# Optimization experiments

Measured on AMD Instinct MI355X. Metric: run time of the kernel, lower is better.

The kernel has to match this reference:

```python
import jax, jax.numpy as jnp
import numpy as np

EMBED_DIM = 1024
N_HEADS = 16


def setup_inputs() -> dict:
    key = jax.random.key(0)
    k1, k2, k3 = jax.random.split(key, 3)
    B, T, C = 4, 2048, EMBED_DIM
    x0 = jax.random.normal(k1, (B, T, C), dtype=jnp.float32)
    # Linear weights stored as (in, out) so y = x @ W, matching torch Linear math.
    w_attn = jax.random.normal(k2, (C, 3 * C), dtype=jnp.float32) * (1.0 / np.sqrt(C))
    w_proj = jax.random.normal(k3, (C, C), dtype=jnp.float32) * (1.0 / np.sqrt(C))
    return {"x0": x0, "w_attn": w_attn, "w_proj": w_proj}


def reference(x0, w_attn, w_proj):
    B, T, C = x0.shape
    H = N_HEADS
    D = C // H  # head dim
    qkv = x0 @ w_attn                      # [B, T, 3C]
    q, k, v = jnp.split(qkv, 3, axis=-1)
    # [B, T, C] -> [B, H, T, D]
    q = q.reshape(B, T, H, D).transpose(0, 2, 1, 3)
    k = k.reshape(B, T, H, D).transpose(0, 2, 1, 3)
    v = v.reshape(B, T, H, D).transpose(0, 2, 1, 3)
    scale = 1.0 / np.sqrt(D)
    attn = jnp.einsum('bhqd,bhkd->bhqk', q, k) * scale  # [B, H, T, T]
    causal = jnp.tril(jnp.ones((T, T), dtype=bool))
    attn = jnp.where(causal[None, None, :, :], attn, -jnp.inf)
    attn = jax.nn.softmax(attn, axis=-1)
    y = jnp.einsum('bhqk,bhkd->bhqd', attn, v)           # [B, H, T, D]
    y = y.transpose(0, 2, 1, 3).reshape(B, T, C)
    return y @ w_proj
```

## Files before the change

kernel.cpp:

```cpp
#include <hip/hip_runtime.h>

#define TSEQ 2048
#define NB 4
#define NH 16
#define HD 64
#define CEMB 1024
#define MROWS (NB*TSEQ)

typedef _Float16 half8 __attribute__((ext_vector_type(8)));
typedef _Float16 half4_t __attribute__((ext_vector_type(4)));
typedef float floatx4 __attribute__((ext_vector_type(4)));

__device__ __forceinline__ floatx4 mfma16x32(half8 a, half8 b, floatx4 c) {
    return __builtin_amdgcn_mfma_f32_16x16x32_f16(a, b, c, 0, 0, 0);
}

__device__ __forceinline__ void async16(const _Float16* g, _Float16* l) {
    __builtin_amdgcn_global_load_lds((const __attribute__((address_space(1))) void*)g,
                                     (__attribute__((address_space(3))) void*)l, 16, 0, 0);
}

__global__ __launch_bounds__(256) void cvt_fp32_fp16(const float* __restrict__ in,
                                                     _Float16* __restrict__ out) {
    size_t i = ((size_t)blockIdx.x * 256 + threadIdx.x) * 8;
    float4 a = *(const float4*)(in + i);
    float4 b = *(const float4*)(in + i + 4);
    half8 h;
    h[0] = (_Float16)a.x; h[1] = (_Float16)a.y; h[2] = (_Float16)a.z; h[3] = (_Float16)a.w;
    h[4] = (_Float16)b.x; h[5] = (_Float16)b.y; h[6] = (_Float16)b.z; h[7] = (_Float16)b.w;
    *(half8*)(out + i) = h;
}

__global__ __launch_bounds__(256) void transpose_cvt(const float* __restrict__ in,
                                                     _Float16* __restrict__ out,
                                                     int R, int Ccols) {
    __shared__ float tile[32][33];
    int bx = blockIdx.x;
    int by = blockIdx.y;
    int tx = threadIdx.x, ty = threadIdx.y;
    int x = bx * 32 + tx;
#pragma unroll
    for (int i = 0; i < 32; i += 8) {
        int y = by * 32 + ty + i;
        tile[ty + i][tx] = in[(size_t)y * Ccols + x];
    }
    __syncthreads();
#pragma unroll
    for (int i = 0; i < 32; i += 8) {
        int oc = bx * 32 + ty + i;
        int orow = by * 32 + tx;
        out[(size_t)oc * R + orow] = (_Float16)tile[tx][ty + i];
    }
}

template<int MODE>
__global__ __launch_bounds__(256, 2) void gemm_w4(const _Float16* __restrict__ A,
                                                  const _Float16* __restrict__ Bt,
                                                  float* __restrict__ Cf,
                                                  _Float16* __restrict__ Ch,
                                                  _Float16* __restrict__ VTh,
                                                  int N, int K) {
    __shared__ __align__(16) _Float16 As[3][128 * 32];
    __shared__ __align__(16) _Float16 Bs[3][256 * 32];

    const int tid = threadIdx.x;
    const int wv = tid >> 6, lane = tid & 63;
    const int l16 = lane & 15, quad = lane >> 4;

    const int pid = blockIdx.x + gridDim.x * blockIdx.y;
    const int nn = gridDim.y;
    const int pig = 8 * nn;
    const int gid = pid / pig;
    const int rem = pid - gid * pig;
    const int bm = gid * 8 + (rem & 7);
    const int bn = rem >> 3;

    const int rA = tid >> 2;
    const int kA = ((tid & 3) ^ ((tid >> 3) & 3)) * 8;
    const _Float16* Ag = A  + (size_t)(bm * 128 + rA) * K + kA;
    const _Float16* Bg = Bt + (size_t)(bn * 256 + rA) * K + kA;

    auto stage = [&](int slot, int ss) {
        const int k0 = ss * 32;
#pragma unroll
        for (int u = 0; u < 2; u++)
            async16(Ag + (size_t)(u * 64) * K + k0, &As[slot][tid * 8 + u * 2048]);
#pragma unroll
        for (int u = 0; u < 4; u++)
            async16(Bg + (size_t)(u * 64) * K + k0, &Bs[slot][tid * 8 + u * 2048]);
    };

    const floatx4 zero = {0.f, 0.f, 0.f, 0.f};
    floatx4 acc[8][4];
#pragma unroll
    for (int i = 0; i < 8; i++)
#pragma unroll
        for (int j = 0; j < 4; j++) acc[i][j] = zero;

    const int sw2 = (quad ^ ((l16 >> 1) & 3)) * 8;
    const int offA = l16 * 32 + sw2;
    const int offB = (wv * 64 + l16) * 32 + sw2;

#define PHASE(s, slot, slot2, STG, WAIT)                                        \
    do {                                                                        \
        if (STG) stage(slot2, (s) + 2);                                         \
        half8 af[8], bf[4];                                                     \
        _Pragma("unroll") for (int i_ = 0; i_ < 8; i_++)                        \
            af[i_] = *(const half8*)&As[slot][offA + i_ * 512];                 \
        _Pragma("unroll") for (int j_ = 0; j_ < 4; j_++)                        \
            bf[j_] = *(const half8*)&Bs[slot][offB + j_ * 512];                 \
        __builtin_amdgcn_s_setprio(1);                                          \
        _Pragma("unroll") for (int i_ = 0; i_ < 8; i_++)                        \
            _Pragma("unroll") for (int j_ = 0; j_ < 4; j_++)                    \
                acc[i_][j_] = mfma16x32(af[i_], bf[j_], acc[i_][j_]);           \
        __builtin_amdgcn_s_setprio(0);                                          \
        if (WAIT == 2)                                                          \
            asm volatile("s_waitcnt vmcnt(6) lgkmcnt(0)\n\ts_barrier" ::: "memory"); \
        else if (WAIT == 1)                                                     \
            asm volatile("s_waitcnt vmcnt(0) lgkmcnt(0)\n\ts_barrier" ::: "memory"); \
        __builtin_amdgcn_sched_barrier(0);                                      \
    } while (0)

    stage(0, 0); stage(1, 1); stage(2, 2);
    asm volatile("s_waitcnt vmcnt(12)\n\ts_barrier" ::: "memory");

    for (int it = 0; it < 10; ++it) {
        const int s0 = it * 3;
        PHASE(s0 + 0, 0, 2, 1, 2);
        PHASE(s0 + 1, 1, 0, 1, 2);
        PHASE(s0 + 2, 2, 1, 1, 2);
    }
    PHASE(30, 0, 0, 0, 1);
    PHASE(31, 1, 0, 0, 0);
#undef PHASE

    if (MODE == 1) {
#pragma unroll
        for (int i = 0; i < 8; i++) {
            int row = bm * 128 + i * 16 + quad * 4;
#pragma unroll
            for (int j = 0; j < 4; j++) {
                int col = bn * 256 + wv * 64 + j * 16 + l16;
#pragma unroll
                for (int r = 0; r < 4; r++)
                    Cf[(size_t)(row + r) * N + col] = acc[i][j][r];
            }
        }
    } else {
        const int which = bn >> 2;
        if (which < 2) {
#pragma unroll
            for (int j = 0; j < 4; j++) {
                int n = bn * 256 + wv * 64 + j * 16 + l16;
                int c = n & 1023, h = c >> 6, d = c & 63;
                _Float16* dst = Ch + (size_t)which * ((size_t)MROWS * CEMB)
                                   + (size_t)h * (TSEQ * HD) + d;
#pragma unroll
                for (int i = 0; i < 8; i++) {
                    int row = bm * 128 + i * 16 + quad * 4;
#pragma unroll
                    for (int r = 0; r < 4; r++) {
                        int m = row + r;
                        int b = m >> 11, t = m & 2047;
                        dst[(size_t)b * (NH * TSEQ * HD) + (size_t)t * HD] = (_Float16)acc[i][j][r];
                    }
                }
            }
        } else {
#pragma unroll
            for (int j = 0; j < 4; j++) {
                int n = bn * 256 + wv * 64 + j * 16 + l16;
                int c = n & 1023, h = c >> 6, d = c & 63;
#pragma unroll
                for (int i = 0; i < 8; i++) {
                    int m0 = bm * 128 + i * 16 + quad * 4;
                    int b = m0 >> 11, t = m0 & 2047;
                    half4_t pk;
#pragma unroll
                    for (int r = 0; r < 4; r++) pk[r] = (_Float16)acc[i][j][r];
                    *(half4_t*)&VTh[(((size_t)(b * NH + h)) * HD + d) * TSEQ + t] = pk;
                }
            }
        }
    }
}

__global__ __launch_bounds__(512, 4) void attn_fwd(const _Float16* __restrict__ Qg,
                                                   const _Float16* __restrict__ Kg,
                                                   const _Float16* __restrict__ VTg,
                                                   _Float16* __restrict__ Y) {
    __shared__ __align__(16) _Float16 Ks[2][4096];
    __shared__ __align__(16) _Float16 Vt[2][4096];

    const int tid = threadIdx.x;
    const int w = tid >> 6, lane = tid & 63;
    const int l16 = lane & 15, quad = lane >> 4;
    const int bh = blockIdx.y;
    const int x = blockIdx.x;
    const int b = bh >> 4, h = bh & 15;
    const int qt = (b < 2) ? x : (7 - x);

    const _Float16* Qb = Qg + (size_t)bh * TSEQ * HD;
    const _Float16* Kb = Kg + (size_t)bh * TSEQ * HD;
    const _Float16* Vb = VTg + (size_t)bh * HD * TSEQ;

    const _Float16 ksc = (_Float16)(0.125f * 1.44269504089f);
    const floatx4 zero = {0.f, 0.f, 0.f, 0.f};

    half8 qf[2][2];
#pragma unroll
    for (int g = 0; g < 2; g++) {
        const _Float16* qrow = Qb + (size_t)(qt * 256 + g * 128 + w * 16 + l16) * HD;
        qf[g][0] = *(const half8*)(qrow + quad * 8);
        qf[g][1] = *(const half8*)(qrow + 32 + quad * 8);
#pragma unroll
        for (int e = 0; e < 8; e++) { qf[g][0][e] *= ksc; qf[g][1][e] *= ksc; }
    }

    floatx4 o[2][4];
#pragma unroll
    for (int g = 0; g < 2; g++)
#pragma unroll
        for (int dt = 0; dt < 4; dt++) o[g][dt] = zero;
    float lsum[2] = {0.f, 0.f};

    const int srow8 = lane >> 3;
    const int scol8 = ((lane & 7) ^ (lane >> 3)) * 8;

    auto stage = [&](int bf, int kt2) {
        const int row = w * 8 + srow8;
        async16(Kb + (size_t)(kt2 * 64 + row) * HD + scol8, &Ks[bf][w * 512]);
        async16(Vb + (size_t)row * TSEQ + kt2 * 64 + scol8, &Vt[bf][w * 512]);
    };

    const int kmax = 4 * qt + 3;
    stage(0, 0);
    int buf = 0;
    for (int kt = 0; kt <= kmax; ++kt) {
        __syncthreads();
        if (kt < kmax) stage(buf ^ 1, kt + 1);

        half8 kf0[4], kf1[4];
#pragma unroll
        for (int nj = 0; nj < 4; nj++) {
            const int rb = (nj * 16 + l16) * 64;
            kf0[nj] = *(const half8*)&Ks[buf][rb + ((quad ^ (l16 & 7)) * 8)];
            kf1[nj] = *(const half8*)&Ks[buf][rb + (((quad ^ 4) ^ (l16 & 7)) * 8)];
        }

        const bool doA = (kt <= 4 * qt + 1);
        half8 pf[2][2];
#pragma unroll
        for (int g = 0; g < 2; g++) {
            if (g == 0 && !doA) continue;
            floatx4 st[4];
#pragma unroll
            for (int nj = 0; nj < 4; nj++) {
                floatx4 t = mfma16x32(kf0[nj], qf[g][0], zero);
                st[nj] = mfma16x32(kf1[nj], qf[g][1], t);
            }
            if (kt * 64 + 63 > qt * 256 + g * 128 + w * 16) {
                const int klim = qt * 256 + g * 128 + w * 16 + l16 - kt * 64;
#pragma unroll
                for (int nj = 0; nj < 4; nj++)
#pragma unroll
                    for (int r = 0; r < 4; r++) {
                        int key = nj * 16 + quad * 4 + r;
                        if (key > klim) st[nj][r] = -1e30f;
                    }
            }
#pragma unroll
            for (int nj = 0; nj < 4; nj++)
#pragma unroll
                for (int r = 0; r < 4; r++) {
                    float p = __builtin_amdgcn_exp2f(st[nj][r]);
                    lsum[g] += p;
                    pf[g][nj >> 1][(nj & 1) * 4 + r] = (_Float16)p;
                }
        }

#pragma unroll
        for (int u = 0; u < 2; u++) {
#pragma unroll
            for (int dt = 0; dt < 4; dt++) {
                const int rb = (dt * 16 + l16) * 64;
                const int g0 = u * 4 + (quad >> 1);
                const int sub = (quad & 1) * 4;
                half4_t lo = *(const half4_t*)&Vt[buf][rb + ((g0 ^ (l16 & 7)) * 8 + sub)];
                half4_t hi = *(const half4_t*)&Vt[buf][rb + (((g0 + 2) ^ (l16 & 7)) * 8 + sub)];
                half8 vf;
                vf[0] = lo[0]; vf[1] = lo[1]; vf[2] = lo[2]; vf[3] = lo[3];
                vf[4] = hi[0]; vf[5] = hi[1]; vf[6] = hi[2]; vf[7] = hi[3];
                if (doA) o[0][dt] = mfma16x32(pf[0][u], vf, o[0][dt]);
                o[1][dt] = mfma16x32(pf[1][u], vf, o[1][dt]);
            }
        }
        buf ^= 1;
    }

#pragma unroll
    for (int g = 0; g < 2; g++) {
        float lt = lsum[g];
        lt += __shfl_xor(lt, 16);
        lt += __shfl_xor(lt, 32);
        float linv[4];
#pragma unroll
        for (int r = 0; r < 4; r++) linv[r] = 1.0f / __shfl(lt, quad * 4 + r);
#pragma unroll
        for (int dt = 0; dt < 4; dt++)
#pragma unroll
            for (int r = 0; r < 4; r++) {
                int q = qt * 256 + g * 128 + w * 16 + quad * 4 + r;
                int d = dt * 16 + l16;
                Y[((size_t)(b * TSEQ + q)) * CEMB + h * HD + d] = (_Float16)(o[g][dt][r] * linv[r]);
            }
    }
}

extern "C" void kernel_launch(void* const* d_in, const int* in_sizes, int n_in,
                              void* d_out, int out_size, void* d_ws, size_t ws_size,
                              hipStream_t stream) {
    const float* x0     = (const float*)d_in[0];
    const float* w_attn = (const float*)d_in[1];
    const float* w_proj = (const float*)d_in[2];
    float* out = (float*)d_out;

    _Float16* xh  = (_Float16*)d_ws;
    _Float16* wqt = xh  + (size_t)MROWS * CEMB;
    _Float16* wpt = wqt + (size_t)3 * CEMB * CEMB;
    _Float16* qh  = wpt + (size_t)CEMB * CEMB;
    _Float16* kh  = qh  + (size_t)MROWS * CEMB;
    _Float16* vt  = kh  + (size_t)MROWS * CEMB;
    _Float16* yh  = vt  + (size_t)MROWS * CEMB;

    cvt_fp32_fp16<<<(MROWS * CEMB) / (256 * 8), 256, 0, stream>>>(x0, xh);
    transpose_cvt<<<dim3(3 * CEMB / 32, CEMB / 32), dim3(32, 8), 0, stream>>>(w_attn, wqt, CEMB, 3 * CEMB);
    transpose_cvt<<<dim3(CEMB / 32, CEMB / 32), dim3(32, 8), 0, stream>>>(w_proj, wpt, CEMB, CEMB);

    gemm_w4<0><<<dim3(MROWS / 128, 3 * CEMB / 256), 256, 0, stream>>>(xh, wqt, nullptr, qh, vt, 3 * CEMB, CEMB);
    attn_fwd<<<dim3(TSEQ / 256, NB * NH), 512, 0, stream>>>(qh, kh, vt, yh);
    gemm_w4<1><<<dim3(MROWS / 128, CEMB / 256), 256, 0, stream>>>(yh, wpt, out, nullptr, nullptr, CEMB, CEMB);
}
```

Baseline: 245.9 us.

## Add 256x256-tile 8-wave QKV GEMM with ping-pong LDS schedule

Replaces the 128x256 four-wave QKV projection GEMM with a new 256x256-tile kernel using 512 threads, a K-step of 64, XOR-swizzled LDS and a four-phase schedule. The schedule interleaves async global-to-LDS loads with MFMA quadrants under explicit barriers and s_setprio. The larger tile is meant to raise arithmetic intensity and cut global/LDS traffic per FLOP. In exchange it uses more LDS and registers, launches fewer blocks (384), and carries hand-tuned waitcnt logic that is fragile.

```diff
diff --git a/kernel.cpp b/kernel.cpp
--- a/kernel.cpp
+++ b/kernel.cpp
@@ -50,6 +50,163 @@
         int oc = bx * 32 + ty + i;
         int orow = by * 32 + tx;
         out[(size_t)oc * R + orow] = (_Float16)tile[tx][ty + i];
+    }
+}
+
+__global__ __launch_bounds__(512, 2) void gemm256(const _Float16* __restrict__ A,
+                                                  const _Float16* __restrict__ Bt,
+                                                  _Float16* __restrict__ Ch,
+                                                  _Float16* __restrict__ VTh,
+                                                  int N, int K) {
+    __shared__ __align__(16) _Float16 Ah[2][2][8192];
+    __shared__ __align__(16) _Float16 Bh[2][2][8192];
+
+    const int tid = threadIdx.x;
+    const int wv = tid >> 6, lane = tid & 63;
+    const int wm = wv >> 2, wn = wv & 3;
+    const int wnh = wn >> 1, wnl = wn & 1;
+    const int l16 = lane & 15, quad = lane >> 4;
+    const int l7 = l16 & 7;
+
+    const int pid = blockIdx.x + gridDim.x * blockIdx.y;
+    const int nn = gridDim.y;
+    const int pig = 8 * nn;
+    const int gid = pid / pig;
+    const int rem = pid - gid * pig;
+    const int bm = gid * 8 + (rem & 7);
+    const int bn = rem >> 3;
+
+    const int rS = tid >> 3;
+    const int kS = ((tid & 7) ^ (rS & 7)) * 8;
+    const _Float16* Asrc = A  + (size_t)(bm * 256 + rS) * K + kS;
+    const _Float16* Bsrc = Bt + (size_t)(bn * 256 + rS) * K + kS;
+
+    auto stA = [&](int d, int mh, int tt) {
+        const _Float16* s = Asrc + (size_t)(mh * 128) * K + tt * 64;
+        async16(s, &Ah[d][mh][wv * 512]);
+        async16(s + (size_t)64 * K, &Ah[d][mh][4096 + wv * 512]);
+    };
+    auto stB = [&](int d, int nh, int tt) {
+        const _Float16* s = Bsrc + (size_t)(nh * 128) * K + tt * 64;
+        async16(s, &Bh[d][nh][wv * 512]);
+        async16(s + (size_t)64 * K, &Bh[d][nh][4096 + wv * 512]);
+    };
+
+    const floatx4 zero = {0.f, 0.f, 0.f, 0.f};
+    floatx4 acc[8][4];
+#pragma unroll
+    for (int i = 0; i < 8; i++)
+#pragma unroll
+        for (int j = 0; j < 4; j++) acc[i][j] = zero;
+
+    const int sw0 = (quad ^ l7) * 8;
+    const int aoff = l16 * 64 + sw0;
+    const int boff = (wnl * 64 + l16) * 64 + sw0;
+
+    half8 af[4][2];
+    half8 bf[2][2][2];
+
+#define RD_A(mq)                                                              \
+    _Pragma("unroll") for (int i_ = 0; i_ < 4; i_++) {                        \
+        af[i_][0] = *(const half8*)&Ac[(mq)*4096 + (aoff + i_*1024)];         \
+        af[i_][1] = *(const half8*)&Ac[(mq)*4096 + ((aoff + i_*1024) ^ 32)];  \
+    }
+#define RD_B(nq)                                                              \
+    _Pragma("unroll") for (int j_ = 0; j_ < 2; j_++) {                        \
+        bf[nq][j_][0] = *(const half8*)&Bc[(nq)*2048 + (boff + j_*1024)];     \
+        bf[nq][j_][1] = *(const half8*)&Bc[(nq)*2048 + ((boff + j_*1024) ^ 32)]; \
+    }
+#define MFMA_Q(mq, nq)                                                        \
+    do {                                                                      \
+        __builtin_amdgcn_s_setprio(1);                                        \
+        _Pragma("unroll") for (int i_ = 0; i_ < 4; i_++)                      \
+            _Pragma("unroll") for (int j_ = 0; j_ < 2; j_++) {                \
+                acc[(mq)*4+i_][(nq)*2+j_] =                                   \
+                    mfma16x32(af[i_][0], bf[nq][j_][0], acc[(mq)*4+i_][(nq)*2+j_]); \
+                acc[(mq)*4+i_][(nq)*2+j_] =                                   \
+                    mfma16x32(af[i_][1], bf[nq][j_][1], acc[(mq)*4+i_][(nq)*2+j_]); \
+            }                                                                 \
+        __builtin_amdgcn_s_setprio(0);                                        \
+    } while (0)
+#define ENDP()                                                                \
+    asm volatile("s_waitcnt lgkmcnt(0)\n\ts_barrier" ::: "memory");           \
+    __builtin_amdgcn_sched_barrier(0)
+
+    stA(0, 0, 0); stA(0, 1, 0); stB(0, 0, 0); stB(0, 1, 0);
+    stA(1, 0, 1); stA(1, 1, 1);
+    asm volatile("s_waitcnt vmcnt(4)\n\ts_barrier" ::: "memory");
+
+    for (int t = 0; t < 16; ++t) {
+        const int d = t & 1;
+        const _Float16* Ac = &Ah[d][wm][0];
+        const _Float16* Bc = &Bh[d][wnh][0];
+
+        RD_A(0); RD_B(0);
+        if (t + 1 < 16) stB(d ^ 1, 0, t + 1);
+        asm volatile("s_barrier" ::: "memory");
+        MFMA_Q(0, 0);
+        ENDP();
+
+        RD_B(1);
+        if (t + 1 < 16) stB(d ^ 1, 1, t + 1);
+        asm volatile("s_barrier" ::: "memory");
+        MFMA_Q(0, 1);
+        ENDP();
+
+        RD_A(1);
+        asm volatile("s_barrier" ::: "memory");
+        MFMA_Q(1, 0);
+        ENDP();
+
+        if (t + 2 < 16) { stA(d, 0, t + 2); stA(d, 1, t + 2); }
+        asm volatile("s_barrier" ::: "memory");
+        MFMA_Q(1, 1);
+        if (t < 14) {
+            asm volatile("s_waitcnt vmcnt(4) lgkmcnt(0)\n\ts_barrier" ::: "memory");
+        } else if (t == 14) {
+            asm volatile("s_waitcnt vmcnt(0) lgkmcnt(0)\n\ts_barrier" ::: "memory");
+        }
+        __builtin_amdgcn_sched_barrier(0);
+    }
+#undef RD_A
+#undef RD_B
+#undef MFMA_Q
+#undef ENDP
+
+    const int which = bn >> 2;
+    if (which < 2) {
+#pragma unroll
+        for (int j = 0; j < 4; j++) {
+            int n = bn * 256 + wn * 64 + j * 16 + l16;
+            int c = n & 1023, h = c >> 6, dd = c & 63;
+            _Float16* dst = Ch + (size_t)which * ((size_t)MROWS * CEMB)
+                               + (size_t)h * (TSEQ * HD) + dd;
+#pragma unroll
+            for (int i = 0; i < 8; i++) {
+                int row = bm * 256 + wm * 128 + i * 16 + quad * 4;
+#pragma unroll
+                for (int r = 0; r < 4; r++) {
+                    int m = row + r;
+                    int b = m >> 11, tt = m & 2047;
+                    dst[(size_t)b * (NH * TSEQ * HD) + (size_t)tt * HD] = (_Float16)acc[i][j][r];
+                }
+            }
+        }
+    } else {
+#pragma unroll
+        for (int j = 0; j < 4; j++) {
+            int n = bn * 256 + wn * 64 + j * 16 + l16;
+            int c = n & 1023, h = c >> 6, dd = c & 63;
+#pragma unroll
+            for (int i = 0; i < 8; i++) {
+                int m0 = bm * 256 + wm * 128 + i * 16 + quad * 4;
+                int b = m0 >> 11, tt = m0 & 2047;
+                half4_t pk;
+#pragma unroll
+                for (int r = 0; r < 4; r++) pk[r] = (_Float16)acc[i][j][r];
+                *(half4_t*)&VTh[(((size_t)(b * NH + h)) * HD + dd) * TSEQ + tt] = pk;
+            }
+        }
     }
 }
 
@@ -146,42 +303,6 @@
                     Cf[(size_t)(row + r) * N + col] = acc[i][j][r];
             }
         }
-    } else {
-        const int which = bn >> 2;
-        if (which < 2) {
-#pragma unroll
-            for (int j = 0; j < 4; j++) {
-                int n = bn * 256 + wv * 64 + j * 16 + l16;
-                int c = n & 1023, h = c >> 6, d = c & 63;
-                _Float16* dst = Ch + (size_t)which * ((size_t)MROWS * CEMB)
-                                   + (size_t)h * (TSEQ * HD) + d;
-#pragma unroll
-                for (int i = 0; i < 8; i++) {
-                    int row = bm * 128 + i * 16 + quad * 4;
-#pragma unroll
-                    for (int r = 0; r < 4; r++) {
-                        int m = row + r;
-                        int b = m >> 11, t = m & 2047;
-                        dst[(size_t)b * (NH * TSEQ * HD) + (size_t)t * HD] = (_Float16)acc[i][j][r];
-                    }
-                }
-            }
-        } else {
-#pragma unroll
-            for (int j = 0; j < 4; j++) {
-                int n = bn * 256 + wv * 64 + j * 16 + l16;
-                int c = n & 1023, h = c >> 6, d = c & 63;
-#pragma unroll
-                for (int i = 0; i < 8; i++) {
-                    int m0 = bm * 128 + i * 16 + quad * 4;
-                    int b = m0 >> 11, t = m0 & 2047;
-                    half4_t pk;
-#pragma unroll
-                    for (int r = 0; r < 4; r++) pk[r] = (_Float16)acc[i][j][r];
-                    *(half4_t*)&VTh[(((size_t)(b * NH + h)) * HD + d) * TSEQ + t] = pk;
-                }
-            }
-        }
     }
 }
 
@@ -337,7 +458,7 @@
     transpose_cvt<<<dim3(3 * CEMB / 32, CEMB / 32), dim3(32, 8), 0, stream>>>(w_attn, wqt, CEMB, 3 * CEMB);
     transpose_cvt<<<dim3(CEMB / 32, CEMB / 32), dim3(32, 8), 0, stream>>>(w_proj, wpt, CEMB, CEMB);
 
-    gemm_w4<0><<<dim3(MROWS / 128, 3 * CEMB / 256), 256, 0, stream>>>(xh, wqt, nullptr, qh, vt, 3 * CEMB, CEMB);
+    gemm256<<<dim3(MROWS / 256, 3 * CEMB / 256), 512, 0, stream>>>(xh, wqt, qh, vt, 3 * CEMB, CEMB);
     attn_fwd<<<dim3(TSEQ / 256, NB * NH), 512, 0, stream>>>(qh, kh, vt, yh);
     gemm_w4<1><<<dim3(MROWS / 128, CEMB / 256), 256, 0, stream>>>(yh, wpt, out, nullptr, nullptr, CEMB, CEMB);
 }
```

New measurement: 252.2 us. +2.6%, slower.
